# Performance work log

Hardware: AMD Instinct MI355X
Metric: run time of the kernel (lower is better)

Reference implementation:

```python
import jax, jax.numpy as jnp
import numpy as np

B, T, V = 512, 400, 32000
ENC, HID, EMB = 1024, 1024, 512


def setup_inputs() -> dict:
    key = jax.random.key(0)
    ks = jax.random.split(key, 10)
    vocab_dist = jax.random.uniform(ks[0], (B, V), dtype=jnp.float32)
    vocab_dist = vocab_dist / vocab_dist.sum(-1, keepdims=True)
    attn_dist = jax.random.uniform(ks[1], (B, T), dtype=jnp.float32)
    attn_dist = attn_dist / attn_dist.sum(-1, keepdims=True)
    return {
        "vocab_dist": vocab_dist,
        "attn_dist": attn_dist,
        "context": jax.random.normal(ks[2], (B, ENC), dtype=jnp.float32),
        "state": jax.random.normal(ks[3], (B, HID), dtype=jnp.float32),
        "emb": jax.random.normal(ks[4], (B, EMB), dtype=jnp.float32),
        "src_ids": jax.random.randint(ks[5], (B, T), 0, 32200),
        "vocab_size": V,
        # learned params: w_c: Linear(enc,1), w_s: Linear(hid,1), w_y: Linear(emb,1), bias b
        "w_c": jax.random.normal(ks[6], (ENC,), dtype=jnp.float32) / np.sqrt(ENC),
        "w_s": jax.random.normal(ks[7], (HID,), dtype=jnp.float32) / np.sqrt(HID),
        "w_y": jax.random.normal(ks[8], (EMB,), dtype=jnp.float32) / np.sqrt(EMB),
        "b": jnp.zeros((1,), dtype=jnp.float32),
    }


def reference(vocab_dist, attn_dist, context, state, emb, src_ids, vocab_size, w_c, w_s, w_y, b):
    # p_gen: [B, 1] gating scalar per batch row
    p_gen = jax.nn.sigmoid(
        (context @ w_c + state @ w_s + emb @ w_y)[:, None] + b
    )
    p_vocab = p_gen * vocab_dist                      # [B, V]
    p_copy = (1.0 - p_gen) * attn_dist                # [B, T]
    copy_mask = (src_ids < vocab_size).astype(p_copy.dtype)
    safe_src_ids = jnp.minimum(src_ids, vocab_size - 1)
    rows = jnp.arange(src_ids.shape[0])[:, None]      # [B, 1]
    final_dist = p_vocab.at[rows, safe_src_ids].add(p_copy * copy_mask)
    return final_dist
```

## Files before the change

### kernel.cpp

```cpp
#include <hip/hip_runtime.h>


#define BLK 256

__global__ __launch_bounds__(BLK) void pg_fused_kernel(
    const float* __restrict__ vocab_dist,
    const float* __restrict__ attn_dist,
    const float* __restrict__ context,
    const float* __restrict__ state,
    const float* __restrict__ emb,
    const int*   __restrict__ src_ids,
    const int*   __restrict__ vocab_size_p,
    const float* __restrict__ w_c,
    const float* __restrict__ w_s,
    const float* __restrict__ w_y,
    const float* __restrict__ bias,
    float* __restrict__ out,
    int T, int V, int ENC, int HID, int EMB)
{
    const int row = blockIdx.x;
    const int tid = threadIdx.x;

    float acc = 0.f;
    {
        const float4* a4 = (const float4*)(context + (size_t)row * ENC);
        const float4* w4 = (const float4*)w_c;
        for (int i = tid; i < (ENC >> 2); i += BLK) {
            float4 a = a4[i], w = w4[i];
            acc += a.x * w.x + a.y * w.y + a.z * w.z + a.w * w.w;
        }
    }
    {
        const float4* a4 = (const float4*)(state + (size_t)row * HID);
        const float4* w4 = (const float4*)w_s;
        for (int i = tid; i < (HID >> 2); i += BLK) {
            float4 a = a4[i], w = w4[i];
            acc += a.x * w.x + a.y * w.y + a.z * w.z + a.w * w.w;
        }
    }
    {
        const float4* a4 = (const float4*)(emb + (size_t)row * EMB);
        const float4* w4 = (const float4*)w_y;
        for (int i = tid; i < (EMB >> 2); i += BLK) {
            float4 a = a4[i], w = w4[i];
            acc += a.x * w.x + a.y * w.y + a.z * w.z + a.w * w.w;
        }
    }

    #pragma unroll
    for (int off = 32; off > 0; off >>= 1)
        acc += __shfl_down(acc, off, 64);

    __shared__ float red[BLK / 64];
    __shared__ float s_pgen;
    if ((tid & 63) == 0) red[tid >> 6] = acc;
    __syncthreads();
    if (tid == 0) {
        float s = red[0] + red[1] + red[2] + red[3] + bias[0];
        s_pgen = 1.f / (1.f + expf(-s));
    }
    __syncthreads();
    const float pg = s_pgen;

    const size_t rowV = (size_t)row * V;
    const float4* vd4 = (const float4*)(vocab_dist + rowV);
    float4*       o4  = (float4*)(out + rowV);
    const int nv4 = V >> 2;
    for (int i = tid; i < nv4; i += BLK) {
        float4 v = vd4[i];
        v.x *= pg; v.y *= pg; v.z *= pg; v.w *= pg;
        o4[i] = v;
    }
    for (int i = (nv4 << 2) + tid; i < V; i += BLK)
        out[rowV + i] = vocab_dist[rowV + i] * pg;

    __syncthreads();

    const int   vs = *vocab_size_p;
    const float pc = 1.f - pg;
    const float* at = attn_dist + (size_t)row * T;
    const int*   si = src_ids  + (size_t)row * T;
    float* orow = out + rowV;
    for (int t = tid; t < T; t += BLK) {
        int id = si[t];
        if (id < vs) atomicAdd(orow + id, pc * at[t]);
    }
}

extern "C" void kernel_launch(void* const* d_in, const int* in_sizes, int n_in,
                              void* d_out, int out_size, void* d_ws, size_t ws_size,
                              hipStream_t stream) {
    const float* vocab_dist = (const float*)d_in[0];
    const float* attn_dist  = (const float*)d_in[1];
    const float* context    = (const float*)d_in[2];
    const float* state      = (const float*)d_in[3];
    const float* emb        = (const float*)d_in[4];
    const int*   src_ids    = (const int*)d_in[5];
    const int*   vocab_sz   = (const int*)d_in[6];
    const float* w_c        = (const float*)d_in[7];
    const float* w_s        = (const float*)d_in[8];
    const float* w_y        = (const float*)d_in[9];
    const float* bias       = (const float*)d_in[10];
    float* out = (float*)d_out;

    const int ENC = in_sizes[7];
    const int HID = in_sizes[8];
    const int EMB = in_sizes[9];
    const int B   = in_sizes[2] / ENC;
    const int T   = in_sizes[1] / B;
    const int V   = in_sizes[0] / B;

    pg_fused_kernel<<<B, BLK, 0, stream>>>(
        vocab_dist, attn_dist, context, state, emb, src_ids, vocab_sz,
        w_c, w_s, w_y, bias, out, T, V, ENC, HID, EMB);
}
```

Measured before the change: 142.7 us.

## Split fused pointer-generator kernel into gate, scale and scatter kernels

Replaces the single per-row fused kernel with three launches: a gate kernel that writes p_gen per row to workspace, a 2D-grid scale kernel that spreads each row's vocab multiply across many blocks, and a 2D-grid scatter kernel for the copy atomics. The intent is to raise parallelism in the bandwidth-bound scale pass beyond one block per row. The cost is two extra launches and a workspace round trip for p_gen.

After: 145.8 us. 2.2% more time.

```diff
diff --git a/kernel.cpp b/kernel.cpp
--- a/kernel.cpp
+++ b/kernel.cpp
@@ -1,31 +1,22 @@
 #include <hip/hip_runtime.h>
 
 
-#define BLK 256
-
-__global__ __launch_bounds__(BLK) void pg_fused_kernel(
-    const float* __restrict__ vocab_dist,
-    const float* __restrict__ attn_dist,
+__global__ __launch_bounds__(256) void pg_gate_kernel(
     const float* __restrict__ context,
     const float* __restrict__ state,
     const float* __restrict__ emb,
-    const int*   __restrict__ src_ids,
-    const int*   __restrict__ vocab_size_p,
-    const float* __restrict__ w_c,
-    const float* __restrict__ w_s,
-    const float* __restrict__ w_y,
-    const float* __restrict__ bias,
-    float* __restrict__ out,
-    int T, int V, int ENC, int HID, int EMB)
+    const float* __restrict__ w_c, const float* __restrict__ w_s,
+    const float* __restrict__ w_y, const float* __restrict__ bias,
+    float* __restrict__ pg,
+    int ENC, int HID, int EMB)
 {
     const int row = blockIdx.x;
     const int tid = threadIdx.x;
-
     float acc = 0.f;
     {
         const float4* a4 = (const float4*)(context + (size_t)row * ENC);
         const float4* w4 = (const float4*)w_c;
-        for (int i = tid; i < (ENC >> 2); i += BLK) {
+        for (int i = tid; i < (ENC >> 2); i += 256) {
             float4 a = a4[i], w = w4[i];
             acc += a.x * w.x + a.y * w.y + a.z * w.z + a.w * w.w;
         }
@@ -33,7 +24,7 @@
     {
         const float4* a4 = (const float4*)(state + (size_t)row * HID);
         const float4* w4 = (const float4*)w_s;
-        for (int i = tid; i < (HID >> 2); i += BLK) {
+        for (int i = tid; i < (HID >> 2); i += 256) {
             float4 a = a4[i], w = w4[i];
             acc += a.x * w.x + a.y * w.y + a.z * w.z + a.w * w.w;
         }
@@ -41,50 +32,62 @@
     {
         const float4* a4 = (const float4*)(emb + (size_t)row * EMB);
         const float4* w4 = (const float4*)w_y;
-        for (int i = tid; i < (EMB >> 2); i += BLK) {
+        for (int i = tid; i < (EMB >> 2); i += 256) {
             float4 a = a4[i], w = w4[i];
             acc += a.x * w.x + a.y * w.y + a.z * w.z + a.w * w.w;
         }
     }
-
     #pragma unroll
     for (int off = 32; off > 0; off >>= 1)
         acc += __shfl_down(acc, off, 64);
-
-    __shared__ float red[BLK / 64];
-    __shared__ float s_pgen;
+    __shared__ float red[4];
     if ((tid & 63) == 0) red[tid >> 6] = acc;
     __syncthreads();
     if (tid == 0) {
         float s = red[0] + red[1] + red[2] + red[3] + bias[0];
-        s_pgen = 1.f / (1.f + expf(-s));
+        pg[row] = 1.f / (1.f + expf(-s));
     }
-    __syncthreads();
-    const float pg = s_pgen;
+}
 
+__global__ __launch_bounds__(256) void pg_scale_kernel(
+    const float* __restrict__ vocab_dist,
+    const float* __restrict__ pg,
+    float* __restrict__ out,
+    int V)
+{
+    const int row = blockIdx.y;
+    const float p = pg[row];
     const size_t rowV = (size_t)row * V;
-    const float4* vd4 = (const float4*)(vocab_dist + rowV);
-    float4*       o4  = (float4*)(out + rowV);
     const int nv4 = V >> 2;
-    for (int i = tid; i < nv4; i += BLK) {
-        float4 v = vd4[i];
-        v.x *= pg; v.y *= pg; v.z *= pg; v.w *= pg;
-        o4[i] = v;
+    const int i4 = blockIdx.x * 256 + threadIdx.x;
+    if (i4 < nv4) {
+        float4 v = ((const float4*)(vocab_dist + rowV))[i4];
+        v.x *= p; v.y *= p; v.z *= p; v.w *= p;
+        ((float4*)(out + rowV))[i4] = v;
     }
-    for (int i = (nv4 << 2) + tid; i < V; i += BLK)
-        out[rowV + i] = vocab_dist[rowV + i] * pg;
+    const int tail = V & 3;
+    if (blockIdx.x == 0 && threadIdx.x < tail) {
+        const int idx = (nv4 << 2) + threadIdx.x;
+        out[rowV + idx] = vocab_dist[rowV + idx] * p;
+    }
+}
 
-    __syncthreads();
-
-    const int   vs = *vocab_size_p;
-    const float pc = 1.f - pg;
-    const float* at = attn_dist + (size_t)row * T;
-    const int*   si = src_ids  + (size_t)row * T;
-    float* orow = out + rowV;
-    for (int t = tid; t < T; t += BLK) {
-        int id = si[t];
-        if (id < vs) atomicAdd(orow + id, pc * at[t]);
-    }
+__global__ __launch_bounds__(256) void pg_scatter_kernel(
+    const float* __restrict__ attn_dist,
+    const int*   __restrict__ src_ids,
+    const int*   __restrict__ vocab_size_p,
+    const float* __restrict__ pg,
+    float* __restrict__ out,
+    int T, int V)
+{
+    const int row = blockIdx.y;
+    const int t = blockIdx.x * 256 + threadIdx.x;
+    if (t >= T) return;
+    const int vs = *vocab_size_p;
+    const float pc = 1.f - pg[row];
+    const int id = src_ids[(size_t)row * T + t];
+    if (id < vs)
+        atomicAdd(out + (size_t)row * V + id, pc * attn_dist[(size_t)row * T + t]);
 }
 
 extern "C" void kernel_launch(void* const* d_in, const int* in_sizes, int n_in,
@@ -102,6 +105,7 @@
     const float* w_y        = (const float*)d_in[9];
     const float* bias       = (const float*)d_in[10];
     float* out = (float*)d_out;
+    float* pg  = (float*)d_ws;
 
     const int ENC = in_sizes[7];
     const int HID = in_sizes[8];
@@ -109,8 +113,16 @@
     const int B   = in_sizes[2] / ENC;
     const int T   = in_sizes[1] / B;
     const int V   = in_sizes[0] / B;
+    const int nv4 = V >> 2;
 
-    pg_fused_kernel<<<B, BLK, 0, stream>>>(
-        vocab_dist, attn_dist, context, state, emb, src_ids, vocab_sz,
-        w_c, w_s, w_y, bias, out, T, V, ENC, HID, EMB);
+    pg_gate_kernel<<<B, 256, 0, stream>>>(context, state, emb,
+                                          w_c, w_s, w_y, bias, pg,
+                                          ENC, HID, EMB);
+
+    dim3 g2((nv4 + 255) / 256, B);
+    pg_scale_kernel<<<g2, 256, 0, stream>>>(vocab_dist, pg, out, V);
+
+    dim3 g3((T + 255) / 256, B);
+    pg_scatter_kernel<<<g3, 256, 0, stream>>>(attn_dist, src_ids, vocab_sz,
+                                              pg, out, T, V);
 }
```
